# Kernel optimization log

Hardware: AMD Instinct MI355X
Metric: run time of the kernel (lower is better)

## Reference

```python
import jax, jax.numpy as jnp
import numpy as np

ALPHA = 0.2  # leaky_relu negative slope
NEG_INF = -1e9


def setup_inputs() -> dict:
    key = jax.random.key(0)
    ks = jax.random.split(key, 8)
    B, U, N, Din, H, HD = 8, 1024, 2048, 128, 4, 32
    return {
        "user_features": jax.random.normal(ks[0], (B, U, Din), jnp.float32),
        "news_features": jax.random.normal(ks[1], (B, N, Din), jnp.float32),
        "adjacency": jax.random.randint(ks[2], (B, U + N, U + N), 0, 2, jnp.int32),
        "W_user": jax.random.normal(ks[3], (H, Din, HD), jnp.float32) * 0.1,
        "W_news": jax.random.normal(ks[4], (H, Din, HD), jnp.float32) * 0.1,
        "a_user_news": jax.random.normal(ks[5], (H, 2 * HD, 1), jnp.float32) * 0.1,
        "a_news_user": jax.random.normal(ks[6], (H, 2 * HD, 1), jnp.float32) * 0.1,
        "b_user": jnp.zeros((H * HD,), jnp.float32),
        "b_news": jnp.zeros((H * HD,), jnp.float32),
    }


def _attention(q, k, a, mask):
    # q: (B,H,Q,hd), k: (B,H,K,hd), a: (H,2*hd,1), mask: (B,Q,K)
    # Additive score decomposed: [q;k] @ a == q@a_q + k@a_k (same math,
    # avoids materializing the (B,H,Q,K,2hd) concat tensor).
    hd = q.shape[-1]
    a_q = a[:, :hd, 0]  # (H,hd)
    a_k = a[:, hd:, 0]  # (H,hd)
    e_q = jnp.einsum("bhqd,hd->bhq", q, a_q)
    e_k = jnp.einsum("bhkd,hd->bhk", k, a_k)
    scores = e_q[..., :, None] + e_k[..., None, :]  # (B,H,Q,K)
    scores = jnp.where(scores > 0, scores, ALPHA * scores)  # leaky_relu
    scores = jnp.where(mask[:, None, :, :] > 0, scores, NEG_INF)
    return jax.nn.softmax(scores, axis=-1)


def reference(user_features, news_features, adjacency, W_user, W_news,
              a_user_news, a_news_user, b_user, b_news):
    B, U, _ = user_features.shape
    N = news_features.shape[1]
    units = b_user.shape[0]
    user_to_news = adjacency[:, :U, U:]   # (B,U,N)
    news_to_user = adjacency[:, U:, :U]   # (B,N,U)

    q_user = jnp.einsum("bud,hdk->bhuk", user_features, W_user)  # (B,H,U,hd)
    k_news = jnp.einsum("bnd,hdk->bhnk", news_features, W_news)  # (B,H,N,hd)

    attn_un = _attention(q_user, k_news, a_user_news, user_to_news)  # (B,H,U,N)
    user_updates = jnp.einsum("bhun,bhnk->bhuk", attn_un, k_news)

    attn_nu = _attention(k_news, q_user, a_news_user, news_to_user)  # (B,H,N,U)
    news_updates = jnp.einsum("bhnu,bhuk->bhnk", attn_nu, q_user)

    # concat_heads=True: original does a raw reshape of (B,H,*,hd) -> (B,*,units)
    updated_users = jnp.reshape(user_updates, (B, U, units)) + b_user
    updated_news = jnp.reshape(news_updates, (B, N, units)) + b_news
    updated_users = jax.nn.relu(updated_users)
    updated_news = jax.nn.relu(updated_news)
    return updated_users, updated_news
```

## Files before the change

kernel.cpp:

```cpp
#include <hip/hip_runtime.h>
#include <hip/hip_bf16.h>

typedef _Float16 half8 __attribute__((ext_vector_type(8)));
typedef __fp16 fp16x2 __attribute__((ext_vector_type(2)));
typedef float f32x4 __attribute__((ext_vector_type(4)));

#define B_ 8
#define U_ 1024
#define N_ 2048
#define DIN 128
#define H_ 4
#define HD 32
#define S_ 3072
#define LOG2E 1.44269504f
#define NU (B_ * U_ * 128)

__global__ __launch_bounds__(256) void p0_kernel(
    const int* __restrict__ adj,
    unsigned int* __restrict__ mA, unsigned int* __restrict__ mB)
{
  const int task = blockIdx.x * 4 + (threadIdx.x >> 6);
  const int l = threadIdx.x & 63;
  const int* rowp;
  unsigned int* mOut;
  int iters;
  if (task < 8192) {
    int b = task >> 10, r = task & 1023;
    rowp = adj + ((size_t)b * S_ + r) * S_ + U_;
    iters = 32;
    mOut = mA + ((size_t)(b * 64 + (r >> 4)) * 64) * 16 + (r & 15);
  } else {
    int t2 = task - 8192;
    int b = t2 >> 11, r = t2 & 2047;
    rowp = adj + ((size_t)b * S_ + U_ + r) * S_;
    iters = 16;
    mOut = mB + ((size_t)(b * 128 + (r >> 4)) * 32) * 16 + (r & 15);
  }
  #pragma unroll 4
  for (int it = 0; it < iters; ++it) {
    int av = rowp[it * 64 + l];
    unsigned long long m = __ballot(av != 0);
    if (l == 0) {
      mOut[(2 * it) * 16]     = (unsigned int)m;
      mOut[(2 * it + 1) * 16] = (unsigned int)(m >> 32);
    }
  }
}

__global__ __launch_bounds__(256) void p1_kernel(
    const float* __restrict__ uf, const float* __restrict__ nf,
    const float* __restrict__ Wu, const float* __restrict__ Wn,
    const float* __restrict__ a_un, const float* __restrict__ a_nu,
    _Float16* __restrict__ vtA, _Float16* __restrict__ vtB,
    float* __restrict__ eRowA, float* __restrict__ eColA,
    float* __restrict__ eRowB, float* __restrict__ eColB)
{
  __shared__ float fs[64][132];
  __shared__ float WsT[32][132];
  __shared__ float qt[32][65];
  __shared__ float aAs[32], aBs[32];

  const int bid = blockIdx.x;
  const int tid = threadIdx.x;

  int b, rt, R, h;
  const float *feat, *W;
  _Float16* vt;
  float *eA, *eB;
  int aAoff, aBoff;
  const float *avA, *avB;
  if (bid < 512) {
    h = bid & 3; int t2 = bid >> 2; b = t2 >> 4; rt = t2 & 15; R = U_;
    feat = uf; W = Wu; vt = vtB;
    eA = eRowA; eB = eColB;
    avA = a_un; aAoff = 0;  avB = a_nu; aBoff = HD;
  } else {
    int t3 = bid - 512;
    h = t3 & 3; int t2 = t3 >> 2; b = t2 >> 5; rt = t2 & 31; R = N_;
    feat = nf; W = Wn; vt = vtA;
    eA = eColA; eB = eRowB;
    avA = a_un; aAoff = HD; avB = a_nu; aBoff = 0;
  }
  const int r0 = rt * 64;

  const float4* feat4 = (const float4*)(feat + ((size_t)b * R + r0) * DIN);
  #pragma unroll
  for (int i = 0; i < 8; ++i) {
    int f4 = tid + 256 * i;
    int row = f4 >> 5, c4 = f4 & 31;
    *(float4*)&fs[row][c4 * 4] = feat4[row * 32 + c4];
  }
  {
    const float4* W4 = (const float4*)(W + (size_t)h * DIN * HD);
    #pragma unroll
    for (int i = 0; i < 4; ++i) {
      int f4 = tid + 256 * i;
      int d = f4 >> 3, kc = f4 & 7;
      float4 v = W4[f4];
      WsT[kc * 4 + 0][d] = v.x;
      WsT[kc * 4 + 1][d] = v.y;
      WsT[kc * 4 + 2][d] = v.z;
      WsT[kc * 4 + 3][d] = v.w;
    }
    if (tid < 32) {
      aAs[tid] = avA[h * 64 + aAoff + tid];
      aBs[tid] = avB[h * 64 + aBoff + tid];
    }
  }
  __syncthreads();

  const int kk = tid & 15, uu = tid >> 4;
  {
    float acc0[4] = {0.f, 0.f, 0.f, 0.f}, acc1[4] = {0.f, 0.f, 0.f, 0.f};
    #pragma unroll 8
    for (int d = 0; d < DIN; d += 4) {
      float4 w0 = *(const float4*)&WsT[kk][d];
      float4 w1 = *(const float4*)&WsT[kk + 16][d];
      #pragma unroll
      for (int i = 0; i < 4; ++i) {
        float4 fv = *(const float4*)&fs[uu + 16 * i][d];
        acc0[i] = fmaf(fv.x, w0.x, acc0[i]); acc0[i] = fmaf(fv.y, w0.y, acc0[i]);
        acc0[i] = fmaf(fv.z, w0.z, acc0[i]); acc0[i] = fmaf(fv.w, w0.w, acc0[i]);
        acc1[i] = fmaf(fv.x, w1.x, acc1[i]); acc1[i] = fmaf(fv.y, w1.y, acc1[i]);
        acc1[i] = fmaf(fv.z, w1.z, acc1[i]); acc1[i] = fmaf(fv.w, w1.w, acc1[i]);
      }
    }
    #pragma unroll
    for (int i = 0; i < 4; ++i) {
      qt[kk][uu + 16 * i] = acc0[i];
      qt[kk + 16][uu + 16 * i] = acc1[i];
    }
  }
  __syncthreads();

  const int u2 = tid & 63, part = tid >> 6;
  {
    size_t vtbase = (size_t)(b * H_ + h) * (R * HD)
                  + (size_t)((r0 >> 5) + (u2 >> 5)) * (HD * 32) + (u2 & 31);
    #pragma unroll
    for (int jj = 0; jj < 8; ++jj) {
      int krow = part * 8 + jj;
      vt[vtbase + krow * 32] = (_Float16)qt[krow][u2];
    }
  }
  if (part < 2) {
    float a_ = 0.f;
    const float* av = (part == 0) ? aAs : aBs;
    #pragma unroll
    for (int k2 = 0; k2 < HD; ++k2)
      a_ = fmaf(qt[k2][u2], av[k2], a_);
    float* e = (part == 0) ? eA : eB;
    e[(size_t)(b * H_ + h) * R + r0 + u2] = a_ * LOG2E;
  }
}

__global__ __launch_bounds__(256) void p2_kernel(
    const unsigned int* __restrict__ mA, const unsigned int* __restrict__ mB,
    const _Float16* __restrict__ vtA, const _Float16* __restrict__ vtB,
    const float* __restrict__ eRowA, const float* __restrict__ eColA,
    const float* __restrict__ eRowB, const float* __restrict__ eColB,
    const float* __restrict__ bu, const float* __restrict__ bn,
    float* __restrict__ numA, float* __restrict__ denA,
    float* __restrict__ out)
{
  const int tid = threadIdx.x;
  const int h = tid >> 6, l = tid & 63;
  const int row16 = l & 15;
  const int cg = (l >> 4) << 3;
  const int bid = blockIdx.x;

  f32x4 acc0 = {0.f,0.f,0.f,0.f}, acc1 = {0.f,0.f,0.f,0.f}, accd = {0.f,0.f,0.f,0.f};
  half8 ones = {(_Float16)1.f, (_Float16)1.f, (_Float16)1.f, (_Float16)1.f,
                (_Float16)1.f, (_Float16)1.f, (_Float16)1.f, (_Float16)1.f};

  const float* ecolH;
  const _Float16* vtb;
  const unsigned int* mT;
  float eq;
  int t0;
  if (bid < 1024) {
    const int b = bid & 7, rest = bid >> 3;
    const int rt = rest & 63, g = rest >> 6;
    eq = eRowA[(size_t)(b * H_ + h) * U_ + rt * 16 + row16];
    ecolH = eColA + (size_t)(b * H_ + h) * N_;
    vtb = vtA + (size_t)(b * H_ + h) * (N_ * HD);
    mT = mA + ((size_t)(b * 64 + rt) * 64) * 16;
    t0 = g * 32;
  } else {
    const int t2 = bid - 1024;
    const int b = t2 & 7, rt = t2 >> 3;
    eq = eRowB[(size_t)(b * H_ + h) * N_ + rt * 16 + row16];
    ecolH = eColB + (size_t)(b * H_ + h) * U_;
    vtb = vtB + (size_t)(b * H_ + h) * (U_ * HD);
    mT = mB + ((size_t)(b * 128 + rt) * 32) * 16;
    t0 = 0;
  }

  #pragma unroll 2
  for (int tt = 0; tt < 32; ++tt) {
    const int t = t0 + tt;
    const int cb = t * 32 + cg;
    unsigned int mb = mT[t * 16 + row16] >> cg;
    float4 e0 = *(const float4*)(ecolH + cb);
    float4 e1 = *(const float4*)(ecolH + cb + 4);
    float ecv[8] = {e0.x, e0.y, e0.z, e0.w, e1.x, e1.y, e1.z, e1.w};
    float wv[8];
    #pragma unroll
    for (int j = 0; j < 8; ++j) {
      float s  = eq + ecv[j];
      float ls = fmaxf(s, 0.2f * s);
      ls = (mb & (1u << j)) ? ls : -1e9f;
      wv[j] = exp2f(ls);
    }
    union { fp16x2 h2[4]; half8 h8; } uw;
    uw.h2[0] = __builtin_amdgcn_cvt_pkrtz(wv[0], wv[1]);
    uw.h2[1] = __builtin_amdgcn_cvt_pkrtz(wv[2], wv[3]);
    uw.h2[2] = __builtin_amdgcn_cvt_pkrtz(wv[4], wv[5]);
    uw.h2[3] = __builtin_amdgcn_cvt_pkrtz(wv[6], wv[7]);
    half8 w = uw.h8;
    const half8 v0 = *(const half8*)(vtb + t * (HD * 32) + row16 * 32 + cg);
    const half8 v1 = *(const half8*)(vtb + t * (HD * 32) + (row16 + 16) * 32 + cg);
    acc0 = __builtin_amdgcn_mfma_f32_16x16x32_f16(w, v0, acc0, 0, 0, 0);
    acc1 = __builtin_amdgcn_mfma_f32_16x16x32_f16(w, v1, acc1, 0, 0, 0);
    accd = __builtin_amdgcn_mfma_f32_16x16x32_f16(w, ones, accd, 0, 0, 0);
  }

  const int colk = row16;
  const int g4 = (l >> 4) << 2;
  if (bid < 1024) {
    const int b = bid & 7, rest = bid >> 3;
    const int rt = rest & 63, g = rest >> 6;
    #pragma unroll
    for (int q = 0; q < 4; ++q) {
      int orow = rt * 16 + g4 + q;
      size_t o = (((size_t)(g * 8 + b) * H_ + h) * U_ + orow) * 32 + colk;
      numA[o] = acc0[q];
      numA[o + 16] = acc1[q];
      if (colk == 0) denA[((size_t)(g * 8 + b) * H_ + h) * U_ + orow] = accd[q];
    }
  } else {
    const int t2 = bid - 1024;
    const int b = t2 & 7, rt = t2 >> 3;
    #pragma unroll
    for (int q = 0; q < 4; ++q) {
      int orow = rt * 16 + g4 + q;
      size_t o = ((size_t)(b * H_ + h) * N_ + orow) * 32 + colk;
      float den = accd[q];
      float v0 = acc0[q] / den + bn[q * 32 + colk];
      float v1 = acc1[q] / den + bn[q * 32 + colk + 16];
      out[NU + o]      = v0 > 0.f ? v0 : 0.f;
      out[NU + o + 16] = v1 > 0.f ? v1 : 0.f;
    }
  }
}

__global__ __launch_bounds__(256) void p3_kernel(
    const float* __restrict__ numA, const float* __restrict__ denA,
    const float* __restrict__ bu, float* __restrict__ out)
{
  int idx = blockIdx.x * 256 + threadIdx.x;
  float n = numA[idx] + numA[idx + NU];
  int dr = idx >> 5;
  float d = denA[dr] + denA[dr + B_ * H_ * U_];
  float v = n / d + bu[idx & 127];
  out[idx] = v > 0.f ? v : 0.f;
}

extern "C" void kernel_launch(void* const* d_in, const int* in_sizes, int n_in,
                              void* d_out, int out_size, void* d_ws, size_t ws_size,
                              hipStream_t stream) {
  const float* uf  = (const float*)d_in[0];
  const float* nf  = (const float*)d_in[1];
  const int*   adj = (const int*)d_in[2];
  const float* Wu  = (const float*)d_in[3];
  const float* Wn  = (const float*)d_in[4];
  const float* aun = (const float*)d_in[5];
  const float* anu = (const float*)d_in[6];
  const float* bu  = (const float*)d_in[7];
  const float* bn  = (const float*)d_in[8];

  char* ws = (char*)d_ws;
  size_t off = 0;
  _Float16* vtA = (_Float16*)(ws + off); off += (size_t)B_ * H_ * HD * N_ * 2;
  _Float16* vtB = (_Float16*)(ws + off); off += (size_t)B_ * H_ * HD * U_ * 2;
  float* eRowA = (float*)(ws + off); off += (size_t)B_ * H_ * U_ * 4;
  float* eColA = (float*)(ws + off); off += (size_t)B_ * H_ * N_ * 4;
  float* eRowB = (float*)(ws + off); off += (size_t)B_ * H_ * N_ * 4;
  float* eColB = (float*)(ws + off); off += (size_t)B_ * H_ * U_ * 4;
  unsigned int* mA = (unsigned int*)(ws + off); off += (size_t)B_ * 64 * 64 * 16 * 4;
  unsigned int* mB = (unsigned int*)(ws + off); off += (size_t)B_ * 128 * 32 * 16 * 4;
  float* numA = (float*)(ws + off); off += (size_t)2 * NU * 4;
  float* denA = (float*)(ws + off); off += (size_t)2 * B_ * H_ * U_ * 4;
  (void)off; (void)ws_size; (void)in_sizes; (void)n_in; (void)out_size;

  p0_kernel<<<6144, 256, 0, stream>>>(adj, mA, mB);
  p1_kernel<<<512 + 1024, 256, 0, stream>>>(uf, nf, Wu, Wn, aun, anu,
                                            vtA, vtB, eRowA, eColA, eRowB, eColB);
  p2_kernel<<<2048, 256, 0, stream>>>(mA, mB, vtA, vtB, eRowA, eColA,
                                      eRowB, eColB, bu, bn, numA, denA, (float*)d_out);
  p3_kernel<<<NU / 256, 256, 0, stream>>>(numA, denA, bu, (float*)d_out);
}
```

Baseline: 122.3 us.

## Regroup p2 blocks by head and stage V tiles through double-buffered LDS

```diff
diff --git a/kernel.cpp b/kernel.cpp
--- a/kernel.cpp
+++ b/kernel.cpp
@@ -154,55 +154,87 @@
   }
 }
 
-__global__ __launch_bounds__(256) void p2_kernel(
+__global__ __launch_bounds__(256, 6) void p2_kernel(
     const unsigned int* __restrict__ mA, const unsigned int* __restrict__ mB,
     const _Float16* __restrict__ vtA, const _Float16* __restrict__ vtB,
     const float* __restrict__ eRowA, const float* __restrict__ eColA,
     const float* __restrict__ eRowB, const float* __restrict__ eColB,
-    const float* __restrict__ bu, const float* __restrict__ bn,
+    const float* __restrict__ bn,
     float* __restrict__ numA, float* __restrict__ denA,
     float* __restrict__ out)
 {
+  __shared__ float eS[1024];
+  __shared__ unsigned int mS[4][32][16];
+  __shared__ char vbufc[2][32 * 80];
+
   const int tid = threadIdx.x;
-  const int h = tid >> 6, l = tid & 63;
+  const int w = tid >> 6, l = tid & 63;
   const int row16 = l & 15;
   const int cg = (l >> 4) << 3;
+
   const int bid = blockIdx.x;
+  int b, h, rg, t0;
+  const _Float16* vtH;
+  const float *ecolH, *erowH;
+  const unsigned int* mRow;
+  const bool isA = (bid < 1024);
+  if (isA) {
+    b = bid & 7; int r1 = bid >> 3; h = r1 & 3; int r2 = r1 >> 2;
+    rg = r2 & 15; int g = r2 >> 4;
+    t0 = g * 32;
+    vtH = vtA + (size_t)(b * H_ + h) * (N_ * HD);
+    ecolH = eColA + (size_t)(b * H_ + h) * N_;
+    erowH = eRowA + (size_t)(b * H_ + h) * U_;
+    mRow = mA + ((size_t)(b * 64 + rg * 4 + w) * 64 + t0) * 16;
+  } else {
+    int t2 = bid - 1024;
+    b = t2 & 7; int r1 = t2 >> 3; h = r1 & 3; rg = r1 >> 2;
+    t0 = 0;
+    vtH = vtB + (size_t)(b * H_ + h) * (U_ * HD);
+    ecolH = eColB + (size_t)(b * H_ + h) * U_;
+    erowH = eRowB + (size_t)(b * H_ + h) * N_;
+    mRow = mB + ((size_t)(b * 128 + rg * 4 + w) * 32) * 16;
+  }
+
+  unsigned int* mf = &mS[0][0][0];
+  {
+    float4 ev = *(const float4*)(ecolH + t0 * 32 + tid * 4);
+    *(float4*)&eS[tid * 4] = ev;
+    int4 m0 = *(const int4*)(mRow + l * 8);
+    int4 m1 = *(const int4*)(mRow + l * 8 + 4);
+    *(int4*)(mf + w * 512 + l * 8) = m0;
+    *(int4*)(mf + w * 512 + l * 8 + 4) = m1;
+  }
+  const int srow = l >> 2, sch = l & 3;
+  const int soff0 = srow * 80 + sch * 16;
+  const int soff1 = (srow + 16) * 80 + sch * 16;
+  if (w == 0) {
+    const char* gsrc = (const char*)(vtH + (size_t)t0 * 1024);
+    int4 pa = *(const int4*)(gsrc + l * 16);
+    int4 pb = *(const int4*)(gsrc + 1024 + l * 16);
+    *(int4*)&vbufc[0][soff0] = pa;
+    *(int4*)&vbufc[0][soff1] = pb;
+  }
+  __syncthreads();
+
+  const float eq = erowH[rg * 64 + w * 16 + row16];
 
   f32x4 acc0 = {0.f,0.f,0.f,0.f}, acc1 = {0.f,0.f,0.f,0.f}, accd = {0.f,0.f,0.f,0.f};
   half8 ones = {(_Float16)1.f, (_Float16)1.f, (_Float16)1.f, (_Float16)1.f,
                 (_Float16)1.f, (_Float16)1.f, (_Float16)1.f, (_Float16)1.f};
 
-  const float* ecolH;
-  const _Float16* vtb;
-  const unsigned int* mT;
-  float eq;
-  int t0;
-  if (bid < 1024) {
-    const int b = bid & 7, rest = bid >> 3;
-    const int rt = rest & 63, g = rest >> 6;
-    eq = eRowA[(size_t)(b * H_ + h) * U_ + rt * 16 + row16];
-    ecolH = eColA + (size_t)(b * H_ + h) * N_;
-    vtb = vtA + (size_t)(b * H_ + h) * (N_ * HD);
-    mT = mA + ((size_t)(b * 64 + rt) * 64) * 16;
-    t0 = g * 32;
-  } else {
-    const int t2 = bid - 1024;
-    const int b = t2 & 7, rt = t2 >> 3;
-    eq = eRowB[(size_t)(b * H_ + h) * N_ + rt * 16 + row16];
-    ecolH = eColB + (size_t)(b * H_ + h) * U_;
-    vtb = vtB + (size_t)(b * H_ + h) * (U_ * HD);
-    mT = mB + ((size_t)(b * 128 + rt) * 32) * 16;
-    t0 = 0;
-  }
-
   #pragma unroll 2
-  for (int tt = 0; tt < 32; ++tt) {
-    const int t = t0 + tt;
-    const int cb = t * 32 + cg;
-    unsigned int mb = mT[t * 16 + row16] >> cg;
-    float4 e0 = *(const float4*)(ecolH + cb);
-    float4 e1 = *(const float4*)(ecolH + cb + 4);
+  for (int t = 0; t < 32; ++t) {
+    const bool more = (t < 31);
+    int4 pa, pb;
+    if (w == 0 && more) {
+      const char* gsrc = (const char*)(vtH + (size_t)(t0 + t + 1) * 1024);
+      pa = *(const int4*)(gsrc + l * 16);
+      pb = *(const int4*)(gsrc + 1024 + l * 16);
+    }
+    unsigned int mb = mf[w * 512 + t * 16 + row16] >> cg;
+    float4 e0 = *(const float4*)&eS[t * 32 + cg];
+    float4 e1 = *(const float4*)&eS[t * 32 + cg + 4];
     float ecv[8] = {e0.x, e0.y, e0.z, e0.w, e1.x, e1.y, e1.z, e1.w};
     float wv[8];
     #pragma unroll
@@ -217,33 +249,39 @@
     uw.h2[1] = __builtin_amdgcn_cvt_pkrtz(wv[2], wv[3]);
     uw.h2[2] = __builtin_amdgcn_cvt_pkrtz(wv[4], wv[5]);
     uw.h2[3] = __builtin_amdgcn_cvt_pkrtz(wv[6], wv[7]);
-    half8 w = uw.h8;
-    const half8 v0 = *(const half8*)(vtb + t * (HD * 32) + row16 * 32 + cg);
-    const half8 v1 = *(const half8*)(vtb + t * (HD * 32) + (row16 + 16) * 32 + cg);
-    acc0 = __builtin_amdgcn_mfma_f32_16x16x32_f16(w, v0, acc0, 0, 0, 0);
-    acc1 = __builtin_amdgcn_mfma_f32_16x16x32_f16(w, v1, acc1, 0, 0, 0);
-    accd = __builtin_amdgcn_mfma_f32_16x16x32_f16(w, ones, accd, 0, 0, 0);
+    half8 wgt = uw.h8;
+    const char* vb = vbufc[t & 1];
+    half8 v0 = *(const half8*)(vb + row16 * 80 + (cg >> 3) * 16);
+    half8 v1 = *(const half8*)(vb + (row16 + 16) * 80 + (cg >> 3) * 16);
+    acc0 = __builtin_amdgcn_mfma_f32_16x16x32_f16(wgt, v0, acc0, 0, 0, 0);
+    acc1 = __builtin_amdgcn_mfma_f32_16x16x32_f16(wgt, v1, acc1, 0, 0, 0);
+    accd = __builtin_amdgcn_mfma_f32_16x16x32_f16(wgt, ones, accd, 0, 0, 0);
+    if (more) {
+      __syncthreads();
+      if (w == 0) {
+        *(int4*)&vbufc[(t + 1) & 1][soff0] = pa;
+        *(int4*)&vbufc[(t + 1) & 1][soff1] = pb;
+      }
+      __syncthreads();
+    }
   }
 
   const int colk = row16;
   const int g4 = (l >> 4) << 2;
-  if (bid < 1024) {
-    const int b = bid & 7, rest = bid >> 3;
-    const int rt = rest & 63, g = rest >> 6;
+  if (isA) {
+    const int g = t0 >> 5;
     #pragma unroll
     for (int q = 0; q < 4; ++q) {
-      int orow = rt * 16 + g4 + q;
+      int orow = rg * 64 + w * 16 + g4 + q;
       size_t o = (((size_t)(g * 8 + b) * H_ + h) * U_ + orow) * 32 + colk;
       numA[o] = acc0[q];
       numA[o + 16] = acc1[q];
       if (colk == 0) denA[((size_t)(g * 8 + b) * H_ + h) * U_ + orow] = accd[q];
     }
   } else {
-    const int t2 = bid - 1024;
-    const int b = t2 & 7, rt = t2 >> 3;
     #pragma unroll
     for (int q = 0; q < 4; ++q) {
-      int orow = rt * 16 + g4 + q;
+      int orow = rg * 64 + w * 16 + g4 + q;
       size_t o = ((size_t)(b * H_ + h) * N_ + orow) * 32 + colk;
       float den = accd[q];
       float v0 = acc0[q] / den + bn[q * 32 + colk];
@@ -297,6 +335,6 @@
   p1_kernel<<<512 + 1024, 256, 0, stream>>>(uf, nf, Wu, Wn, aun, anu,
                                             vtA, vtB, eRowA, eColA, eRowB, eColB);
   p2_kernel<<<2048, 256, 0, stream>>>(mA, mB, vtA, vtB, eRowA, eColA,
-                                      eRowB, eColB, bu, bn, numA, denA, (float*)d_out);
+                                      eRowB, eColB, bn, numA, denA, (float*)d_out);
   p3_kernel<<<NU / 256, 256, 0, stream>>>(numA, denA, bu, (float*)d_out);
 }
```

Result: no change. 120.1 us (-1.8%).

## Merge mask-packing and projection kernels; batch loads two tiles ahead in attention loop

Applied to the files above, without the earlier changes.

```diff
diff --git a/kernel.cpp b/kernel.cpp
--- a/kernel.cpp
+++ b/kernel.cpp
@@ -15,54 +15,53 @@
 #define LOG2E 1.44269504f
 #define NU (B_ * U_ * 128)
 
-__global__ __launch_bounds__(256) void p0_kernel(
+__global__ __launch_bounds__(256) void p01_kernel(
     const int* __restrict__ adj,
-    unsigned int* __restrict__ mA, unsigned int* __restrict__ mB)
-{
-  const int task = blockIdx.x * 4 + (threadIdx.x >> 6);
-  const int l = threadIdx.x & 63;
-  const int* rowp;
-  unsigned int* mOut;
-  int iters;
-  if (task < 8192) {
-    int b = task >> 10, r = task & 1023;
-    rowp = adj + ((size_t)b * S_ + r) * S_ + U_;
-    iters = 32;
-    mOut = mA + ((size_t)(b * 64 + (r >> 4)) * 64) * 16 + (r & 15);
-  } else {
-    int t2 = task - 8192;
-    int b = t2 >> 11, r = t2 & 2047;
-    rowp = adj + ((size_t)b * S_ + U_ + r) * S_;
-    iters = 16;
-    mOut = mB + ((size_t)(b * 128 + (r >> 4)) * 32) * 16 + (r & 15);
-  }
-  #pragma unroll 4
-  for (int it = 0; it < iters; ++it) {
-    int av = rowp[it * 64 + l];
-    unsigned long long m = __ballot(av != 0);
-    if (l == 0) {
-      mOut[(2 * it) * 16]     = (unsigned int)m;
-      mOut[(2 * it + 1) * 16] = (unsigned int)(m >> 32);
-    }
-  }
-}
-
-__global__ __launch_bounds__(256) void p1_kernel(
     const float* __restrict__ uf, const float* __restrict__ nf,
     const float* __restrict__ Wu, const float* __restrict__ Wn,
     const float* __restrict__ a_un, const float* __restrict__ a_nu,
+    unsigned int* __restrict__ mA, unsigned int* __restrict__ mB,
     _Float16* __restrict__ vtA, _Float16* __restrict__ vtB,
     float* __restrict__ eRowA, float* __restrict__ eColA,
     float* __restrict__ eRowB, float* __restrict__ eColB)
 {
+  const int bid0 = blockIdx.x;
+  const int tid = threadIdx.x;
+  if (bid0 < 6144) {
+    const int task = bid0 * 4 + (tid >> 6);
+    const int l = tid & 63;
+    const int* rowp;
+    unsigned int* mOut;
+    int iters;
+    if (task < 8192) {
+      int b = task >> 10, r = task & 1023;
+      rowp = adj + ((size_t)b * S_ + r) * S_ + U_;
+      iters = 32;
+      mOut = mA + ((size_t)(b * 64 + (r >> 4)) * 64) * 16 + (r & 15);
+    } else {
+      int t2 = task - 8192;
+      int b = t2 >> 11, r = t2 & 2047;
+      rowp = adj + ((size_t)b * S_ + U_ + r) * S_;
+      iters = 16;
+      mOut = mB + ((size_t)(b * 128 + (r >> 4)) * 32) * 16 + (r & 15);
+    }
+    #pragma unroll 4
+    for (int it = 0; it < iters; ++it) {
+      int av = rowp[it * 64 + l];
+      unsigned long long m = __ballot(av != 0);
+      if (l == 0) {
+        mOut[(2 * it) * 16]     = (unsigned int)m;
+        mOut[(2 * it + 1) * 16] = (unsigned int)(m >> 32);
+      }
+    }
+    return;
+  }
   __shared__ float fs[64][132];
   __shared__ float WsT[32][132];
   __shared__ float qt[32][65];
   __shared__ float aAs[32], aBs[32];
 
-  const int bid = blockIdx.x;
-  const int tid = threadIdx.x;
-
+  const int bid = bid0 - 6144;
   int b, rt, R, h;
   const float *feat, *W;
   _Float16* vt;
@@ -154,12 +153,37 @@
   }
 }
 
+__device__ __forceinline__ void wgen_mfma(
+    unsigned int mb, float eq, const float4& e0, const float4& e1,
+    const half8& v0, const half8& v1, half8 ones,
+    f32x4& acc0, f32x4& acc1, f32x4& accd)
+{
+  float ecv[8] = {e0.x, e0.y, e0.z, e0.w, e1.x, e1.y, e1.z, e1.w};
+  float wv[8];
+  #pragma unroll
+  for (int j = 0; j < 8; ++j) {
+    float s  = eq + ecv[j];
+    float ls = fmaxf(s, 0.2f * s);
+    ls = (mb & (1u << j)) ? ls : -1e9f;
+    wv[j] = exp2f(ls);
+  }
+  union { fp16x2 h2[4]; half8 h8; } uw;
+  uw.h2[0] = __builtin_amdgcn_cvt_pkrtz(wv[0], wv[1]);
+  uw.h2[1] = __builtin_amdgcn_cvt_pkrtz(wv[2], wv[3]);
+  uw.h2[2] = __builtin_amdgcn_cvt_pkrtz(wv[4], wv[5]);
+  uw.h2[3] = __builtin_amdgcn_cvt_pkrtz(wv[6], wv[7]);
+  half8 w = uw.h8;
+  acc0 = __builtin_amdgcn_mfma_f32_16x16x32_f16(w, v0, acc0, 0, 0, 0);
+  acc1 = __builtin_amdgcn_mfma_f32_16x16x32_f16(w, v1, acc1, 0, 0, 0);
+  accd = __builtin_amdgcn_mfma_f32_16x16x32_f16(w, ones, accd, 0, 0, 0);
+}
+
 __global__ __launch_bounds__(256) void p2_kernel(
     const unsigned int* __restrict__ mA, const unsigned int* __restrict__ mB,
     const _Float16* __restrict__ vtA, const _Float16* __restrict__ vtB,
     const float* __restrict__ eRowA, const float* __restrict__ eColA,
     const float* __restrict__ eRowB, const float* __restrict__ eColB,
-    const float* __restrict__ bu, const float* __restrict__ bn,
+    const float* __restrict__ bn,
     float* __restrict__ numA, float* __restrict__ denA,
     float* __restrict__ out)
 {
@@ -196,33 +220,22 @@
     t0 = 0;
   }
 
-  #pragma unroll 2
-  for (int tt = 0; tt < 32; ++tt) {
-    const int t = t0 + tt;
-    const int cb = t * 32 + cg;
-    unsigned int mb = mT[t * 16 + row16] >> cg;
-    float4 e0 = *(const float4*)(ecolH + cb);
-    float4 e1 = *(const float4*)(ecolH + cb + 4);
-    float ecv[8] = {e0.x, e0.y, e0.z, e0.w, e1.x, e1.y, e1.z, e1.w};
-    float wv[8];
-    #pragma unroll
-    for (int j = 0; j < 8; ++j) {
-      float s  = eq + ecv[j];
-      float ls = fmaxf(s, 0.2f * s);
-      ls = (mb & (1u << j)) ? ls : -1e9f;
-      wv[j] = exp2f(ls);
-    }
-    union { fp16x2 h2[4]; half8 h8; } uw;
-    uw.h2[0] = __builtin_amdgcn_cvt_pkrtz(wv[0], wv[1]);
-    uw.h2[1] = __builtin_amdgcn_cvt_pkrtz(wv[2], wv[3]);
-    uw.h2[2] = __builtin_amdgcn_cvt_pkrtz(wv[4], wv[5]);
-    uw.h2[3] = __builtin_amdgcn_cvt_pkrtz(wv[6], wv[7]);
-    half8 w = uw.h8;
-    const half8 v0 = *(const half8*)(vtb + t * (HD * 32) + row16 * 32 + cg);
-    const half8 v1 = *(const half8*)(vtb + t * (HD * 32) + (row16 + 16) * 32 + cg);
-    acc0 = __builtin_amdgcn_mfma_f32_16x16x32_f16(w, v0, acc0, 0, 0, 0);
-    acc1 = __builtin_amdgcn_mfma_f32_16x16x32_f16(w, v1, acc1, 0, 0, 0);
-    accd = __builtin_amdgcn_mfma_f32_16x16x32_f16(w, ones, accd, 0, 0, 0);
+  for (int tt = 0; tt < 32; tt += 2) {
+    const int ta = t0 + tt, tb = ta + 1;
+    unsigned int mwa = mT[ta * 16 + row16];
+    unsigned int mwb = mT[tb * 16 + row16];
+    const int cba = ta * 32 + cg, cbb = tb * 32 + cg;
+    float4 ea0 = *(const float4*)(ecolH + cba);
+    float4 ea1 = *(const float4*)(ecolH + cba + 4);
+    float4 eb0 = *(const float4*)(ecolH + cbb);
+    float4 eb1 = *(const float4*)(ecolH + cbb + 4);
+    half8 va0 = *(const half8*)(vtb + ta * (HD * 32) + row16 * 32 + cg);
+    half8 va1 = *(const half8*)(vtb + ta * (HD * 32) + (row16 + 16) * 32 + cg);
+    half8 vb0 = *(const half8*)(vtb + tb * (HD * 32) + row16 * 32 + cg);
+    half8 vb1 = *(const half8*)(vtb + tb * (HD * 32) + (row16 + 16) * 32 + cg);
+    __builtin_amdgcn_sched_barrier(0);
+    wgen_mfma(mwa >> cg, eq, ea0, ea1, va0, va1, ones, acc0, acc1, accd);
+    wgen_mfma(mwb >> cg, eq, eb0, eb1, vb0, vb1, ones, acc0, acc1, accd);
   }
 
   const int colk = row16;
@@ -293,10 +306,10 @@
   float* denA = (float*)(ws + off); off += (size_t)2 * B_ * H_ * U_ * 4;
   (void)off; (void)ws_size; (void)in_sizes; (void)n_in; (void)out_size;
 
-  p0_kernel<<<6144, 256, 0, stream>>>(adj, mA, mB);
-  p1_kernel<<<512 + 1024, 256, 0, stream>>>(uf, nf, Wu, Wn, aun, anu,
-                                            vtA, vtB, eRowA, eColA, eRowB, eColB);
+  p01_kernel<<<6144 + 1536, 256, 0, stream>>>(adj, uf, nf, Wu, Wn, aun, anu,
+                                              mA, mB, vtA, vtB,
+                                              eRowA, eColA, eRowB, eColB);
   p2_kernel<<<2048, 256, 0, stream>>>(mA, mB, vtA, vtB, eRowA, eColA,
-                                      eRowB, eColB, bu, bn, numA, denA, (float*)d_out);
+                                      eRowB, eColB, bn, numA, denA, (float*)d_out);
   p3_kernel<<<NU / 256, 256, 0, stream>>>(numA, denA, bu, (float*)d_out);
 }
```

Result: slower. 179.6 us (+46.9%).
